# Performance work log

Hardware: AMD Instinct MI355X
Metric: run time of the kernel (lower is better)

## Reference

```python
import jax, jax.numpy as jnp
import numpy as np

N_NODES = 50000

def _lgconv(x, src, dst, norm):
    # gather-scale-scatter: out[i] = sum_{(j->i)} norm_e * x[j]
    msgs = x[src] * norm[:, None]                      # [E, d]
    return jax.ops.segment_sum(msgs, dst, num_segments=N_NODES)  # [N, d]

def setup_inputs() -> dict:
    key = jax.random.key(0)
    k1, k2 = jax.random.split(key)
    x = jax.random.normal(k1, (N_NODES, 128), dtype=jnp.float32)
    edge_index = jax.random.randint(k2, (2, 600000), 0, N_NODES, dtype=jnp.int64)
    return {"x": x, "edge_index": edge_index}

def reference(x, edge_index):
    src, dst = edge_index[0], edge_index[1]
    # PyG gcn_norm (no self loops, edge_weight = 1):
    deg = jax.ops.segment_sum(jnp.ones_like(src, dtype=x.dtype), dst, num_segments=N_NODES)
    dinv = jnp.where(deg > 0, jax.lax.rsqrt(jnp.where(deg > 0, deg, 1.0)), 0.0)
    norm = dinv[src] * dinv[dst]                       # [E]
    # Three stacked LGConv + relu (dropout is identity in eval mode)
    x = jax.nn.relu(_lgconv(x, src, dst, norm))
    x = jax.nn.relu(_lgconv(x, src, dst, norm))
    x = jax.nn.relu(_lgconv(x, src, dst, norm))
    return x
```

## Files before the change

### kernel.cpp

```cpp
#include <hip/hip_runtime.h>
#include <hip/hip_fp16.h>

#define NN 50000
#define FEAT 128

__global__ void init_kernel(const unsigned int* ei32, int* flag, int* hist, int n) {
    int i = blockIdx.x * 256 + threadIdx.x;
    if (i < n) hist[i] = 0;
    if (blockIdx.x == 0) {
        __shared__ int ok;
        if (threadIdx.x == 0) ok = 1;
        __syncthreads();
        if (ei32[2 * threadIdx.x + 1] != 0u) ok = 0;
        __syncthreads();
        if (threadIdx.x == 0) *flag = ok;
    }
}

static __device__ __forceinline__ void load_edge(const void* ei, int is64, int E, int e,
                                                 int& src, int& dst) {
    if (is64) {
        const long long* p = (const long long*)ei;
        src = (int)p[e];
        dst = (int)p[E + e];
    } else {
        const int* p = (const int*)ei;
        src = p[e];
        dst = p[E + e];
    }
}

__global__ void rank_kernel(const void* ei, const int* flag, int* hist,
                            int* __restrict__ rank, int E) {
    int base = (blockIdx.x * blockDim.x + threadIdx.x) * 4;
    if (base >= E) return;
    const int is64 = *flag;
    int n = E - base; if (n > 4) n = 4;
    int src[4], dst[4];
    #pragma unroll
    for (int i = 0; i < 4; ++i)
        if (i < n) load_edge(ei, is64, E, base + i, src[i], dst[i]);
    int r[4];
    #pragma unroll
    for (int i = 0; i < 4; ++i)
        if (i < n) r[i] = atomicAdd(&hist[dst[i]], 1);
    #pragma unroll
    for (int i = 0; i < 4; ++i)
        if (i < n) rank[base + i] = r[i];
}

__global__ void scan_local_kernel(const int* __restrict__ hist, int* __restrict__ local_excl,
                                  int* __restrict__ bsum, float* __restrict__ dinv, int n) {
    __shared__ int sdata[256];
    int i = blockIdx.x * 256 + threadIdx.x;
    int v = (i < n) ? hist[i] : 0;
    if (i < n) dinv[i] = (v > 0) ? rsqrtf((float)v) : 0.0f;
    sdata[threadIdx.x] = v;
    __syncthreads();
    for (int d = 1; d < 256; d <<= 1) {
        int t = (threadIdx.x >= (unsigned)d) ? sdata[threadIdx.x - d] : 0;
        __syncthreads();
        sdata[threadIdx.x] += t;
        __syncthreads();
    }
    if (i < n) local_excl[i] = sdata[threadIdx.x] - v;
    if (threadIdx.x == 255) bsum[blockIdx.x] = sdata[255];
}

__global__ void scan_bsum_kernel(int* bsum, int nb) {
    __shared__ int sdata[1024];
    int v = ((int)threadIdx.x < nb) ? bsum[threadIdx.x] : 0;
    sdata[threadIdx.x] = v;
    __syncthreads();
    for (int d = 1; d < 1024; d <<= 1) {
        int t = (threadIdx.x >= (unsigned)d) ? sdata[threadIdx.x - d] : 0;
        __syncthreads();
        sdata[threadIdx.x] += t;
        __syncthreads();
    }
    if ((int)threadIdx.x < nb) bsum[threadIdx.x] = sdata[threadIdx.x] - v;
}

__global__ void scan_add_kernel(const int* __restrict__ local_excl, const int* __restrict__ bsum,
                                int* __restrict__ rowp, int n, int E) {
    int i = blockIdx.x * 256 + threadIdx.x;
    if (i < n) rowp[i] = local_excl[i] + bsum[i >> 8];
    if (i == 0) rowp[n] = E;
}

__global__ void place_kernel(const void* ei, const int* flag,
                             const int* __restrict__ rowp, const int* __restrict__ rank,
                             int* __restrict__ col, int E) {
    int base = (blockIdx.x * blockDim.x + threadIdx.x) * 4;
    if (base >= E) return;
    const int is64 = *flag;
    int n = E - base; if (n > 4) n = 4;
    int src[4], dst[4], r[4];
    #pragma unroll
    for (int i = 0; i < 4; ++i)
        if (i < n) { load_edge(ei, is64, E, base + i, src[i], dst[i]); r[i] = rank[base + i]; }
    int rp[4];
    #pragma unroll
    for (int i = 0; i < 4; ++i)
        if (i < n) rp[i] = rowp[dst[i]];
    #pragma unroll
    for (int i = 0; i < 4; ++i)
        if (i < n) __builtin_nontemporal_store(src[i], &col[rp[i] + r[i]]);
}

static __device__ __forceinline__ float4 relu4(float4 v) {
    v.x = fmaxf(v.x, 0.0f); v.y = fmaxf(v.y, 0.0f);
    v.z = fmaxf(v.z, 0.0f); v.w = fmaxf(v.w, 0.0f);
    return v;
}

static __device__ __forceinline__ void fma4(float4& a, float w, float4 v) {
    a.x += w * v.x; a.y += w * v.y; a.z += w * v.z; a.w += w * v.w;
}

static __device__ __forceinline__ float4 h4_to_f4(uint2 r) {
    __half2 lo = *reinterpret_cast<__half2*>(&r.x);
    __half2 hi = *reinterpret_cast<__half2*>(&r.y);
    float2 f0 = __half22float2(lo);
    float2 f1 = __half22float2(hi);
    return make_float4(f0.x, f0.y, f1.x, f1.y);
}

static __device__ __forceinline__ uint2 f4_to_h4(float4 v) {
    __half2 lo = __floats2half2_rn(v.x, v.y);
    __half2 hi = __floats2half2_rn(v.z, v.w);
    uint2 r;
    r.x = *reinterpret_cast<unsigned int*>(&lo);
    r.y = *reinterpret_cast<unsigned int*>(&hi);
    return r;
}

__global__ void cvt_f2h_kernel(const float4* __restrict__ in, const float* __restrict__ dinv,
                               uint2* __restrict__ outh, int n4) {
    int i = blockIdx.x * blockDim.x + threadIdx.x;
    if (i >= n4) return;
    float dd = dinv[i >> 5];
    float4 v = in[i];
    v.x *= dd; v.y *= dd; v.z *= dd; v.w *= dd;
    outh[i] = f4_to_h4(v);
}

template <bool OUT_HALF>
__global__ void conv_h_kernel(const uint2* __restrict__ xh,
                              const int* __restrict__ row_ptr,
                              const int* __restrict__ col,
                              const float* __restrict__ dinv,
                              void* __restrict__ outbuf) {
    int gid = blockIdx.x * blockDim.x + threadIdx.x;
    int node = gid >> 5;
    int f4   = gid & 31;
    if (node >= NN) return;
    int beg = row_ptr[node];
    int end = row_ptr[node + 1];
    float dd = dinv[node];

    float4 a0 = make_float4(0.f, 0.f, 0.f, 0.f);
    float4 a1 = a0, a2 = a0, a3 = a0;

    for (int cb = beg; cb < end; cb += 32) {
        int rem = end - cb;
        if (rem > 32) rem = 32;
        int myi = (f4 < rem) ? f4 : 0;
        int pk = __builtin_nontemporal_load(&col[cb + myi]);

        for (int j = 0; j < rem; j += 8) {
            int i0 = j + 0, i1 = j + 1, i2 = j + 2, i3 = j + 3;
            int i4 = j + 4, i5 = j + 5, i6 = j + 6, i7 = j + 7;
            int last = rem - 1;
            int c0 = __shfl(pk, i0 < rem ? i0 : last, 32);
            int c1 = __shfl(pk, i1 < rem ? i1 : last, 32);
            int c2 = __shfl(pk, i2 < rem ? i2 : last, 32);
            int c3 = __shfl(pk, i3 < rem ? i3 : last, 32);
            int c4 = __shfl(pk, i4 < rem ? i4 : last, 32);
            int c5 = __shfl(pk, i5 < rem ? i5 : last, 32);
            int c6 = __shfl(pk, i6 < rem ? i6 : last, 32);
            int c7 = __shfl(pk, i7 < rem ? i7 : last, 32);

            float w0 = (i0 < rem) ? 1.0f : 0.0f;
            float w1 = (i1 < rem) ? 1.0f : 0.0f;
            float w2 = (i2 < rem) ? 1.0f : 0.0f;
            float w3 = (i3 < rem) ? 1.0f : 0.0f;
            float w4 = (i4 < rem) ? 1.0f : 0.0f;
            float w5 = (i5 < rem) ? 1.0f : 0.0f;
            float w6 = (i6 < rem) ? 1.0f : 0.0f;
            float w7 = (i7 < rem) ? 1.0f : 0.0f;

            uint2 r0 = xh[c0 * 32 + f4];
            uint2 r1 = xh[c1 * 32 + f4];
            uint2 r2 = xh[c2 * 32 + f4];
            uint2 r3 = xh[c3 * 32 + f4];
            uint2 r4 = xh[c4 * 32 + f4];
            uint2 r5 = xh[c5 * 32 + f4];
            uint2 r6 = xh[c6 * 32 + f4];
            uint2 r7 = xh[c7 * 32 + f4];

            fma4(a0, w0, h4_to_f4(r0));
            fma4(a1, w1, h4_to_f4(r1));
            fma4(a2, w2, h4_to_f4(r2));
            fma4(a3, w3, h4_to_f4(r3));
            fma4(a0, w4, h4_to_f4(r4));
            fma4(a1, w5, h4_to_f4(r5));
            fma4(a2, w6, h4_to_f4(r6));
            fma4(a3, w7, h4_to_f4(r7));
        }
    }

    float4 acc;
    acc.x = (a0.x + a1.x) + (a2.x + a3.x);
    acc.y = (a0.y + a1.y) + (a2.y + a3.y);
    acc.z = (a0.z + a1.z) + (a2.z + a3.z);
    acc.w = (a0.w + a1.w) + (a2.w + a3.w);
    acc.x *= dd; acc.y *= dd; acc.z *= dd; acc.w *= dd;
    acc = relu4(acc);

    if (OUT_HALF) {
        acc.x *= dd; acc.y *= dd; acc.z *= dd; acc.w *= dd;
        ((uint2*)outbuf)[node * 32 + f4] = f4_to_h4(acc);
    } else {
        ((float4*)outbuf)[node * 32 + f4] = acc;
    }
}

__global__ void deg_kernel(const void* ei, const int* flag, float* deg, int E) {
    int e = blockIdx.x * blockDim.x + threadIdx.x;
    if (e >= E) return;
    int src, dst;
    load_edge(ei, *flag, E, e, src, dst);
    atomicAdd(&deg[dst], 1.0f);
}

__global__ void dinv_kernel(float* deg) {
    int i = blockIdx.x * blockDim.x + threadIdx.x;
    if (i >= NN) return;
    float d = deg[i];
    deg[i] = (d > 0.0f) ? (1.0f / sqrtf(d)) : 0.0f;
}

template <bool RELU_IN>
__global__ void conv_atomic_kernel(const float* __restrict__ xin, const void* ei, const int* flag,
                                   const float* __restrict__ dinv, float* __restrict__ yout, int E) {
    int gid = blockIdx.x * blockDim.x + threadIdx.x;
    int e  = gid >> 5;
    int f4 = gid & 31;
    if (e >= E) return;
    int src, dst;
    load_edge(ei, *flag, E, e, src, dst);
    float w = dinv[src] * dinv[dst];
    float4 v = ((const float4*)xin)[src * 32 + f4];
    if (RELU_IN) v = relu4(v);
    float* o = yout + (size_t)dst * FEAT + f4 * 4;
    atomicAdd(o + 0, v.x * w);
    atomicAdd(o + 1, v.y * w);
    atomicAdd(o + 2, v.z * w);
    atomicAdd(o + 3, v.w * w);
}

__global__ void relu_kernel(float4* buf, int n4) {
    int i = blockIdx.x * blockDim.x + threadIdx.x;
    if (i >= n4) return;
    buf[i] = relu4(buf[i]);
}

extern "C" void kernel_launch(void* const* d_in, const int* in_sizes, int n_in,
                              void* d_out, int out_size, void* d_ws, size_t ws_size,
                              hipStream_t stream) {
    const float* x  = (const float*)d_in[0];
    const void*  ei = d_in[1];
    const int E = in_sizes[1] / 2;

    float* out = (float*)d_out;
    char*  ws  = (char*)d_ws;

    const size_t feat_bytes  = (size_t)NN * FEAT * sizeof(float);
    const size_t half_bytes  = (size_t)NN * FEAT * sizeof(unsigned short);
    const int NB = (NN + 255) / 256;
    const int N4 = NN * 32;

    const size_t OFF_FLAG = 0;
    const size_t OFF_HIST = 1024;
    const size_t OFF_DINV = OFF_HIST + (((size_t)NN * 4 + 255) & ~255ull);
    const size_t OFF_ROWP = OFF_DINV + (((size_t)NN * 4 + 255) & ~255ull);
    const size_t OFF_BSUM = OFF_ROWP + ((((size_t)NN + 1) * 4 + 255) & ~255ull);
    const size_t OFF_RNK  = OFF_BSUM + ((1024 * 4 + 255) & ~255ull);
    const size_t OFF_COL  = OFF_RNK + (((size_t)E * 4 + 255) & ~255ull);
    const size_t OFF_HA   = OFF_COL + (((size_t)E * 4 + 255) & ~255ull);
    const size_t OFF_HB   = OFF_HA + ((half_bytes + 255) & ~255ull);
    const size_t NEEDED   = OFF_HB + half_bytes;

    int* flag = (int*)(ws + OFF_FLAG);

    if (ws_size >= NEEDED) {
        int*   hist = (int*)(ws + OFF_HIST);
        float* dinv = (float*)(ws + OFF_DINV);
        int*   rowp = (int*)(ws + OFF_ROWP);
        int*   bsum = (int*)(ws + OFF_BSUM);
        int*   rank = (int*)(ws + OFF_RNK);
        int*   col  = (int*)(ws + OFF_COL);
        uint2* hA   = (uint2*)(ws + OFF_HA);
        uint2* hB   = (uint2*)(ws + OFF_HB);

        init_kernel<<<NB, 256, 0, stream>>>((const unsigned int*)ei, flag, hist, NN);

        const int e4_blocks = (E / 4 + 255) / 256 + 1;
        rank_kernel<<<e4_blocks, 256, 0, stream>>>(ei, flag, hist, rank, E);
        scan_local_kernel<<<NB, 256, 0, stream>>>(hist, rowp, bsum, dinv, NN);
        cvt_f2h_kernel<<<(N4 + 255) / 256, 256, 0, stream>>>((const float4*)x, dinv, hA, N4);
        scan_bsum_kernel<<<1, 1024, 0, stream>>>(bsum, NB);
        scan_add_kernel<<<NB, 256, 0, stream>>>(rowp, bsum, rowp, NN, E);
        place_kernel<<<e4_blocks, 256, 0, stream>>>(ei, flag, rowp, rank, col, E);

        const int conv_blocks = (NN * 32 + 255) / 256;
        conv_h_kernel<true><<<conv_blocks, 256, 0, stream>>>(hA, rowp, col, dinv, hB);
        conv_h_kernel<true><<<conv_blocks, 256, 0, stream>>>(hB, rowp, col, dinv, hA);
        conv_h_kernel<false><<<conv_blocks, 256, 0, stream>>>(hA, rowp, col, dinv, out);
    } else {
        float* dinv = (float*)(ws + 1024);
        float* y    = (float*)(ws + 262144);

        hipMemsetAsync(dinv, 0, NN * sizeof(float), stream);
        hipMemsetAsync(out, 0, feat_bytes, stream);
        hipMemsetAsync(y, 0, feat_bytes, stream);

        init_kernel<<<1, 256, 0, stream>>>((const unsigned int*)ei, flag, (int*)(ws + 512), 256);
        deg_kernel<<<(E + 255) / 256, 256, 0, stream>>>(ei, flag, dinv, E);
        dinv_kernel<<<(NN + 255) / 256, 256, 0, stream>>>(dinv);

        const int conv_blocks = (int)(((size_t)E * 32 + 255) / 256);
        conv_atomic_kernel<false><<<conv_blocks, 256, 0, stream>>>(x, ei, flag, dinv, out, E);
        conv_atomic_kernel<true><<<conv_blocks, 256, 0, stream>>>(out, ei, flag, dinv, y, E);
        hipMemsetAsync(out, 0, feat_bytes, stream);
        conv_atomic_kernel<true><<<conv_blocks, 256, 0, stream>>>(y, ei, flag, dinv, out, E);
        relu_kernel<<<(out_size / 4 + 255) / 256, 256, 0, stream>>>((float4*)out, out_size / 4);
    }
}
```

Baseline: 144.7 us.

## Pack edge records into 64-bit words, use 16-bit column indices, fuse scan

The rank kernel now writes one 64-bit record per edge holding src, dst and the atomic rank. The place kernel reads that record instead of re-reading the int64 edge_index plus a separate rank array. Column indices are stored as 16-bit values, which halves the index traffic in the three conv passes. The separate block-sum scan kernel is removed: each scan_add block reduces the preceding block sums itself, saving a launch. This relies on NN fitting in 16 bits (NN is 50000, so it does) and adds a redundant reduction in every block.

```diff
diff --git a/kernel.cpp b/kernel.cpp
--- a/kernel.cpp
+++ b/kernel.cpp
@@ -31,7 +31,7 @@
 }
 
 __global__ void rank_kernel(const void* ei, const int* flag, int* hist,
-                            int* __restrict__ rank, int E) {
+                            unsigned long long* __restrict__ prk, int E) {
     int base = (blockIdx.x * blockDim.x + threadIdx.x) * 4;
     if (base >= E) return;
     const int is64 = *flag;
@@ -46,7 +46,9 @@
         if (i < n) r[i] = atomicAdd(&hist[dst[i]], 1);
     #pragma unroll
     for (int i = 0; i < 4; ++i)
-        if (i < n) rank[base + i] = r[i];
+        if (i < n)
+            prk[base + i] = (unsigned long long)(unsigned int)(src[i] | (dst[i] << 16)) |
+                            ((unsigned long long)(unsigned int)r[i] << 32);
 }
 
 __global__ void scan_local_kernel(const int* __restrict__ hist, int* __restrict__ local_excl,
@@ -67,45 +69,43 @@
     if (threadIdx.x == 255) bsum[blockIdx.x] = sdata[255];
 }
 
-__global__ void scan_bsum_kernel(int* bsum, int nb) {
-    __shared__ int sdata[1024];
-    int v = ((int)threadIdx.x < nb) ? bsum[threadIdx.x] : 0;
+__global__ void scan_add_kernel(const int* __restrict__ local_excl, const int* __restrict__ bsum,
+                                int* __restrict__ rowp, int n, int E) {
+    __shared__ int sdata[256];
+    int b = blockIdx.x;
+    int v = ((int)threadIdx.x < b) ? bsum[threadIdx.x] : 0;
     sdata[threadIdx.x] = v;
     __syncthreads();
-    for (int d = 1; d < 1024; d <<= 1) {
-        int t = (threadIdx.x >= (unsigned)d) ? sdata[threadIdx.x - d] : 0;
-        __syncthreads();
-        sdata[threadIdx.x] += t;
-        __syncthreads();
-    }
-    if ((int)threadIdx.x < nb) bsum[threadIdx.x] = sdata[threadIdx.x] - v;
-}
-
-__global__ void scan_add_kernel(const int* __restrict__ local_excl, const int* __restrict__ bsum,
-                                int* __restrict__ rowp, int n, int E) {
-    int i = blockIdx.x * 256 + threadIdx.x;
-    if (i < n) rowp[i] = local_excl[i] + bsum[i >> 8];
+    for (int d = 128; d > 0; d >>= 1) {
+        if ((int)threadIdx.x < d) sdata[threadIdx.x] += sdata[threadIdx.x + d];
+        __syncthreads();
+    }
+    int off = sdata[0];
+    int i = b * 256 + threadIdx.x;
+    if (i < n) rowp[i] = local_excl[i] + off;
     if (i == 0) rowp[n] = E;
 }
 
-__global__ void place_kernel(const void* ei, const int* flag,
-                             const int* __restrict__ rowp, const int* __restrict__ rank,
-                             int* __restrict__ col, int E) {
+__global__ void place_kernel(const unsigned long long* __restrict__ prk,
+                             const int* __restrict__ rowp,
+                             unsigned short* __restrict__ col, int E) {
     int base = (blockIdx.x * blockDim.x + threadIdx.x) * 4;
     if (base >= E) return;
-    const int is64 = *flag;
     int n = E - base; if (n > 4) n = 4;
-    int src[4], dst[4], r[4];
-    #pragma unroll
-    for (int i = 0; i < 4; ++i)
-        if (i < n) { load_edge(ei, is64, E, base + i, src[i], dst[i]); r[i] = rank[base + i]; }
+    unsigned long long p[4];
+    #pragma unroll
+    for (int i = 0; i < 4; ++i)
+        if (i < n) p[i] = prk[base + i];
     int rp[4];
     #pragma unroll
     for (int i = 0; i < 4; ++i)
-        if (i < n) rp[i] = rowp[dst[i]];
-    #pragma unroll
-    for (int i = 0; i < 4; ++i)
-        if (i < n) __builtin_nontemporal_store(src[i], &col[rp[i] + r[i]]);
+        if (i < n) rp[i] = rowp[(int)((p[i] >> 16) & 0xFFFF)];
+    #pragma unroll
+    for (int i = 0; i < 4; ++i)
+        if (i < n) {
+            int pos = rp[i] + (int)(p[i] >> 32);
+            __builtin_nontemporal_store((unsigned short)(p[i] & 0xFFFF), &col[pos]);
+        }
 }
 
 static __device__ __forceinline__ float4 relu4(float4 v) {
@@ -148,7 +148,7 @@
 template <bool OUT_HALF>
 __global__ void conv_h_kernel(const uint2* __restrict__ xh,
                               const int* __restrict__ row_ptr,
-                              const int* __restrict__ col,
+                              const unsigned short* __restrict__ col,
                               const float* __restrict__ dinv,
                               void* __restrict__ outbuf) {
     int gid = blockIdx.x * blockDim.x + threadIdx.x;
@@ -166,7 +166,7 @@
         int rem = end - cb;
         if (rem > 32) rem = 32;
         int myi = (f4 < rem) ? f4 : 0;
-        int pk = __builtin_nontemporal_load(&col[cb + myi]);
+        int pk = (int)__builtin_nontemporal_load(&col[cb + myi]);
 
         for (int j = 0; j < rem; j += 8) {
             int i0 = j + 0, i1 = j + 1, i2 = j + 2, i3 = j + 3;
@@ -286,9 +286,9 @@
     const size_t OFF_DINV = OFF_HIST + (((size_t)NN * 4 + 255) & ~255ull);
     const size_t OFF_ROWP = OFF_DINV + (((size_t)NN * 4 + 255) & ~255ull);
     const size_t OFF_BSUM = OFF_ROWP + ((((size_t)NN + 1) * 4 + 255) & ~255ull);
-    const size_t OFF_RNK  = OFF_BSUM + ((1024 * 4 + 255) & ~255ull);
-    const size_t OFF_COL  = OFF_RNK + (((size_t)E * 4 + 255) & ~255ull);
-    const size_t OFF_HA   = OFF_COL + (((size_t)E * 4 + 255) & ~255ull);
+    const size_t OFF_PRK  = OFF_BSUM + ((1024 * 4 + 255) & ~255ull);
+    const size_t OFF_COL  = OFF_PRK + (((size_t)E * 8 + 255) & ~255ull);
+    const size_t OFF_HA   = OFF_COL + (((size_t)E * 2 + 255) & ~255ull);
     const size_t OFF_HB   = OFF_HA + ((half_bytes + 255) & ~255ull);
     const size_t NEEDED   = OFF_HB + half_bytes;
 
@@ -299,20 +299,19 @@
         float* dinv = (float*)(ws + OFF_DINV);
         int*   rowp = (int*)(ws + OFF_ROWP);
         int*   bsum = (int*)(ws + OFF_BSUM);
-        int*   rank = (int*)(ws + OFF_RNK);
-        int*   col  = (int*)(ws + OFF_COL);
+        unsigned long long* prk = (unsigned long long*)(ws + OFF_PRK);
+        unsigned short* col = (unsigned short*)(ws + OFF_COL);
         uint2* hA   = (uint2*)(ws + OFF_HA);
         uint2* hB   = (uint2*)(ws + OFF_HB);
 
         init_kernel<<<NB, 256, 0, stream>>>((const unsigned int*)ei, flag, hist, NN);
 
         const int e4_blocks = (E / 4 + 255) / 256 + 1;
-        rank_kernel<<<e4_blocks, 256, 0, stream>>>(ei, flag, hist, rank, E);
+        rank_kernel<<<e4_blocks, 256, 0, stream>>>(ei, flag, hist, prk, E);
         scan_local_kernel<<<NB, 256, 0, stream>>>(hist, rowp, bsum, dinv, NN);
         cvt_f2h_kernel<<<(N4 + 255) / 256, 256, 0, stream>>>((const float4*)x, dinv, hA, N4);
-        scan_bsum_kernel<<<1, 1024, 0, stream>>>(bsum, NB);
         scan_add_kernel<<<NB, 256, 0, stream>>>(rowp, bsum, rowp, NN, E);
-        place_kernel<<<e4_blocks, 256, 0, stream>>>(ei, flag, rowp, rank, col, E);
+        place_kernel<<<e4_blocks, 256, 0, stream>>>(prk, rowp, col, E);
 
         const int conv_blocks = (NN * 32 + 255) / 256;
         conv_h_kernel<true><<<conv_blocks, 256, 0, stream>>>(hA, rowp, col, dinv, hB);
```

Result: no change. 145.1 us (+0.3%).
